# Kernel tuning notes

Measured on AMD Instinct MI355X. Metric: run time of the kernel, lower is better.

## Reference

```python
import jax, jax.numpy as jnp
import numpy as np
import math

E = 64    # d_model = 2*feats
FF = 16   # dim_feedforward
F = 32    # feats
W = 100   # window_size
B = 128   # batch
NH = 32   # nhead = feats


def _mha(q_in, kv_in, w_qkv, b_qkv, w_o, b_o):
    # PyTorch nn.MultiheadAttention, seq-first layout [L, B, E]
    wq, wk, wv = jnp.split(w_qkv, 3, axis=0)
    bq, bk, bv = jnp.split(b_qkv, 3)
    q = q_in @ wq.T + bq
    k = kv_in @ wk.T + bk
    v = kv_in @ wv.T + bv
    L, Bb, _ = q.shape
    S = k.shape[0]
    hd = E // NH  # head_dim = 2
    qh = q.reshape(L, Bb, NH, hd)
    kh = k.reshape(S, Bb, NH, hd)
    vh = v.reshape(S, Bb, NH, hd)
    scores = jnp.einsum('lbhd,sbhd->bhls', qh, kh) / math.sqrt(hd)
    attn = jax.nn.softmax(scores, axis=-1)
    out = jnp.einsum('bhls,sbhd->lbhd', attn, vh).reshape(L, Bb, E)
    return out @ w_o.T + b_o


def _ffn(x, w1, b1, w2, b2):
    h = x @ w1.T + b1
    # nn.LeakyReLU(True) => negative_slope=True==1.0 => identity activation
    return h @ w2.T + b2


def _pos_encode(x):
    # pe[t,d] = sin(t*div[d]) + cos(t*div[d])  (both added, as in source)
    div = jnp.exp(jnp.arange(E, dtype=x.dtype) * (-math.log(10000.0) / E))
    pos = jnp.arange(x.shape[0], dtype=x.dtype)[:, None]
    pe = jnp.sin(pos * div) + jnp.cos(pos * div)  # [W, E]
    return x + pe[:, None, :]


def _encode(src, c, tgt, enc_p):
    (qkv_w, qkv_b, out_w, out_b, l1_w, l1_b, l2_w, l2_b) = enc_p
    s = jnp.concatenate([src, c], axis=2) * math.sqrt(F)
    s = _pos_encode(s)
    s = s + _mha(s, s, qkv_w, qkv_b, out_w, out_b)
    s = s + _ffn(s, l1_w, l1_b, l2_w, l2_b)
    t = jnp.tile(tgt, (1, 1, 2))
    return t, s


def _decode(t, mem, dec_p):
    (sa_qkv_w, sa_qkv_b, sa_out_w, sa_out_b,
     ca_qkv_w, ca_qkv_b, ca_out_w, ca_out_b,
     l1_w, l1_b, l2_w, l2_b) = dec_p
    t = t + _mha(t, t, sa_qkv_w, sa_qkv_b, sa_out_w, sa_out_b)
    t = t + _mha(t, mem, ca_qkv_w, ca_qkv_b, ca_out_w, ca_out_b)
    t = t + _ffn(t, l1_w, l1_b, l2_w, l2_b)
    return t


def _forward(src, tgt,
             enc_qkv_w, enc_qkv_b, enc_out_w, enc_out_b, enc_l1_w, enc_l1_b, enc_l2_w, enc_l2_b,
             d1_sa_qkv_w, d1_sa_qkv_b, d1_sa_out_w, d1_sa_out_b,
             d1_ca_qkv_w, d1_ca_qkv_b, d1_ca_out_w, d1_ca_out_b,
             d1_l1_w, d1_l1_b, d1_l2_w, d1_l2_b,
             d2_sa_qkv_w, d2_sa_qkv_b, d2_sa_out_w, d2_sa_out_b,
             d2_ca_qkv_w, d2_ca_qkv_b, d2_ca_out_w, d2_ca_out_b,
             d2_l1_w, d2_l1_b, d2_l2_w, d2_l2_b,
             fcn_w, fcn_b):
    enc_p = (enc_qkv_w, enc_qkv_b, enc_out_w, enc_out_b, enc_l1_w, enc_l1_b, enc_l2_w, enc_l2_b)
    d1_p = (d1_sa_qkv_w, d1_sa_qkv_b, d1_sa_out_w, d1_sa_out_b,
            d1_ca_qkv_w, d1_ca_qkv_b, d1_ca_out_w, d1_ca_out_b,
            d1_l1_w, d1_l1_b, d1_l2_w, d1_l2_b)
    d2_p = (d2_sa_qkv_w, d2_sa_qkv_b, d2_sa_out_w, d2_sa_out_b,
            d2_ca_qkv_w, d2_ca_qkv_b, d2_ca_out_w, d2_ca_out_b,
            d2_l1_w, d2_l1_b, d2_l2_w, d2_l2_b)
    fcn = lambda x: jax.nn.sigmoid(x @ fcn_w.T + fcn_b)

    c = jnp.zeros_like(src)
    t, mem = _encode(src, c, tgt, enc_p)
    x1 = fcn(_decode(t, mem, d1_p))
    c = (x1 - src) ** 2
    t, mem = _encode(src, c, tgt, enc_p)
    x2 = fcn(_decode(t, mem, d2_p))
    return x1, x2


def setup_inputs() -> dict:
    keys = jax.random.split(jax.random.key(0), 40)
    ki = iter(keys)

    def rn(shape, s=0.05):
        return jax.random.normal(next(ki), shape, dtype=jnp.float32) * s

    inp = {}
    inp['src'] = jax.random.normal(next(ki), (W, B, F), dtype=jnp.float32)
    inp['tgt'] = jax.random.normal(next(ki), (W, B, F), dtype=jnp.float32)
    for pfx in ['enc_', 'd1_sa_', 'd1_ca_', 'd2_sa_', 'd2_ca_']:
        inp[pfx + 'qkv_w'] = rn((3 * E, E))
        inp[pfx + 'qkv_b'] = rn((3 * E,))
        inp[pfx + 'out_w'] = rn((E, E))
        inp[pfx + 'out_b'] = rn((E,))
    for pfx in ['enc_', 'd1_', 'd2_']:
        inp[pfx + 'l1_w'] = rn((FF, E))
        inp[pfx + 'l1_b'] = rn((FF,))
        inp[pfx + 'l2_w'] = rn((E, FF))
        inp[pfx + 'l2_b'] = rn((E,))
    inp['fcn_w'] = rn((F, E))
    inp['fcn_b'] = rn((F,))
    return inp


def reference(src, tgt,
              enc_qkv_w, enc_qkv_b, enc_out_w, enc_out_b, enc_l1_w, enc_l1_b, enc_l2_w, enc_l2_b,
              d1_sa_qkv_w, d1_sa_qkv_b, d1_sa_out_w, d1_sa_out_b,
              d1_ca_qkv_w, d1_ca_qkv_b, d1_ca_out_w, d1_ca_out_b,
              d1_l1_w, d1_l1_b, d1_l2_w, d1_l2_b,
              d2_sa_qkv_w, d2_sa_qkv_b, d2_sa_out_w, d2_sa_out_b,
              d2_ca_qkv_w, d2_ca_qkv_b, d2_ca_out_w, d2_ca_out_b,
              d2_l1_w, d2_l1_b, d2_l2_w, d2_l2_b,
              fcn_w, fcn_b):
    return _forward(src, tgt,
                    enc_qkv_w, enc_qkv_b, enc_out_w, enc_out_b, enc_l1_w, enc_l1_b, enc_l2_w, enc_l2_b,
                    d1_sa_qkv_w, d1_sa_qkv_b, d1_sa_out_w, d1_sa_out_b,
                    d1_ca_qkv_w, d1_ca_qkv_b, d1_ca_out_w, d1_ca_out_b,
                    d1_l1_w, d1_l1_b, d1_l2_w, d1_l2_b,
                    d2_sa_qkv_w, d2_sa_qkv_b, d2_sa_out_w, d2_sa_out_b,
                    d2_ca_qkv_w, d2_ca_qkv_b, d2_ca_out_w, d2_ca_out_b,
                    d2_l1_w, d2_l1_b, d2_l2_w, d2_l2_b,
                    fcn_w, fcn_b)
```

## Files before the change

### kernel.cpp

```cpp
#include <hip/hip_runtime.h>
#include <math.h>


#define TPB 1024
#define RH 50
#define SQ32 5.656854249492381f

#ifndef __has_builtin
#define __has_builtin(x) 0
#endif
#if __has_builtin(__builtin_amdgcn_exp2f)
#define EXP2(x) __builtin_amdgcn_exp2f(x)
#else
#define EXP2(x) exp2f(x)
#endif

typedef float v2f __attribute__((ext_vector_type(2)));
typedef float v4f __attribute__((ext_vector_type(4)));

struct KParams { const void* p[36]; };

template<int K, int MC, int WP>
__device__ __forceinline__ void ldwp(const float* __restrict__ Wt, float* __restrict__ Ws,
                                     int moff, int tid)
{
    for (int i = tid; i < MC * K; i += TPB) {
        int m = i / K, k = i - m * K;
        Ws[k * WP + moff + m] = Wt[i];
    }
}

template<int K, int WP>
__device__ __forceinline__ void gemm_dual24(const float* __restrict__ x0,
                                            const float* __restrict__ x1,
                                            const float* __restrict__ w, v2f acc[4])
{
#pragma unroll 4
    for (int kk = 0; kk < K / 4; ++kk) {
        v4f xa = *reinterpret_cast<const v4f*>(x0 + 4 * kk);
        v4f xb = *reinterpret_cast<const v4f*>(x1 + 4 * kk);
#pragma unroll
        for (int j = 0; j < 4; ++j) {
            v4f wv = *reinterpret_cast<const v4f*>(w + (size_t)(4 * kk + j) * WP);
            v2f xj = {xa[j], xb[j]};
#pragma unroll
            for (int c = 0; c < 4; ++c) {
                v2f wc = {wv[c], wv[c]};
                acc[c] = __builtin_elementwise_fma(xj, wc, acc[c]);
            }
        }
    }
}

template<int K, int WP>
__device__ __forceinline__ void gemm14v(const float* __restrict__ x,
                                        const float* __restrict__ w, float acc[4])
{
#pragma unroll 4
    for (int kk = 0; kk < K / 4; ++kk) {
        v4f xv = *reinterpret_cast<const v4f*>(x + 4 * kk);
#pragma unroll
        for (int j = 0; j < 4; ++j) {
            v4f wv = *reinterpret_cast<const v4f*>(w + (size_t)(4 * kk + j) * WP);
#pragma unroll
            for (int c = 0; c < 4; ++c) acc[c] = fmaf(xv[j], wv[c], acc[c]);
        }
    }
}

__device__ __forceinline__ void kv_gemm(const float* __restrict__ Xkv,
    const float* __restrict__ RW, const float* __restrict__ Bqkv,
    int b, int base, float4* __restrict__ KVs, float4* __restrict__ Gx, int tid)
{
    if (tid >= 800) return;
    const int isV = tid >= 400;
    const int u = tid - (isV ? 400 : 0);
    const int r0 = u >> 4, cg = u & 15;
    v2f acc[4] = {};
    gemm_dual24<64, 132>(Xkv + r0 * 68, Xkv + (r0 + 25) * 68,
                         RW + (isV ? 64 : 0) + 4 * cg, acc);
    v4f bb = *reinterpret_cast<const v4f*>(Bqkv + (isV ? 128 : 64) + 4 * cg);
    const int h0 = 2 * cg;
    const int off = isV ? 2 : 0;
#pragma unroll
    for (int rr = 0; rr < 2; ++rr) {
        int sg = base + r0 + 25 * rr;
        v2f p0 = {acc[0][rr] + bb[0], acc[1][rr] + bb[1]};
        v2f p1 = {acc[2][rr] + bb[2], acc[3][rr] + bb[3]};
        *reinterpret_cast<v2f*>(reinterpret_cast<float*>(KVs + h0 * 101 + sg) + off) = p0;
        *reinterpret_cast<v2f*>(reinterpret_cast<float*>(KVs + (h0 + 1) * 101 + sg) + off) = p1;
        float* g0 = reinterpret_cast<float*>(Gx + ((size_t)b * 100 + sg) * 32 + h0) + off;
        float* g1 = reinterpret_cast<float*>(Gx + ((size_t)b * 100 + sg) * 32 + h0 + 1) + off;
        asm volatile("global_store_dwordx2 %0, %1, off sc0 sc1" :: "v"(g0), "v"(p0) : "memory");
        asm volatile("global_store_dwordx2 %0, %1, off sc0 sc1" :: "v"(g1), "v"(p1) : "memory");
    }
}

__device__ __forceinline__ void flag_pub(int* flagme, int st, int tid)
{
    asm volatile("s_waitcnt vmcnt(0)" ::: "memory");
    __syncthreads();
    if (tid == 0)
        asm volatile("global_store_dword %0, %1, off sc0 sc1" :: "v"(flagme), "v"(st) : "memory");
}

__device__ __forceinline__ void q_gemm(const float* __restrict__ Xq,
    const float* __restrict__ RW, const float* __restrict__ Bqkv,
    float* __restrict__ Q, int tid)
{
    if (tid >= 400) return;
    const int r0 = tid >> 4, cg = tid & 15;
    v2f acc[4] = {};
    gemm_dual24<64, 132>(Xq + r0 * 68, Xq + (r0 + 25) * 68, RW + 4 * cg, acc);
    v4f bb = *reinterpret_cast<const v4f*>(Bqkv + 4 * cg);
#pragma unroll
    for (int rr = 0; rr < 2; ++rr)
        *reinterpret_cast<v4f*>(Q + (r0 + 25 * rr) * 68 + 4 * cg) =
            (v4f){acc[0][rr] + bb[0], acc[1][rr] + bb[1],
                  acc[2][rr] + bb[2], acc[3][rr] + bb[3]};
}

__device__ __forceinline__ void kv_wait(const int* flagpt, int st,
    const float4* __restrict__ Gx, int b, int pbase,
    float4* __restrict__ KVs, int tid)
{
    if (tid == 0) {
        int f;
        for (;;) {
            asm volatile("global_load_dword %0, %1, off sc0 sc1\n\ts_waitcnt vmcnt(0)"
                         : "=v"(f) : "v"(flagpt) : "memory");
            if (f >= st) break;
            __builtin_amdgcn_s_sleep(8);
        }
    }
    __syncthreads();
    const int i2 = tid + 1024;
    v4f a1, a2;
    const float4* p1 = Gx + ((size_t)b * 100 + pbase + (tid >> 5)) * 32 + (tid & 31);
    asm volatile("global_load_dwordx4 %0, %1, off sc0 sc1" : "=v"(a1) : "v"(p1) : "memory");
    if (i2 < 1600) {
        const float4* p2 = Gx + ((size_t)b * 100 + pbase + (i2 >> 5)) * 32 + (i2 & 31);
        asm volatile("global_load_dwordx4 %0, %1, off sc0 sc1" : "=v"(a2) : "v"(p2) : "memory");
    }
    asm volatile("s_waitcnt vmcnt(0)" ::: "memory");
    *reinterpret_cast<v4f*>(KVs + (tid & 31) * 101 + pbase + (tid >> 5)) = a1;
    if (i2 < 1600)
        *reinterpret_cast<v4f*>(KVs + (i2 & 31) * 101 + pbase + (i2 >> 5)) = a2;
    __syncthreads();
}

__device__ __forceinline__ void attn_block(float* __restrict__ Q,
                                           const float4* __restrict__ KVs, int tid)
{
    if (tid < 832) {
        const int u = tid >> 1, sh = tid & 1;
        const int h = u / 13;
        const int g = u - 13 * h;
        const int lq0 = 4 * g;
        const float4* kv = KVs + h * 101 + sh * 50;
        const float SCALE = 0.7071067811865476f * 1.4426950408889634f;
        float q0[4], q1[4];
#pragma unroll
        for (int j = 0; j < 4; ++j) {
            if (lq0 + j < RH) {
                float2 qv = *reinterpret_cast<const float2*>(Q + (lq0 + j) * 68 + 2 * h);
                q0[j] = qv.x * SCALE; q1[j] = qv.y * SCALE;
            } else { q0[j] = 0.f; q1[j] = 0.f; }
        }
        float mx[4] = {-1e30f, -1e30f, -1e30f, -1e30f};
#pragma unroll 5
        for (int s = 0; s < 50; ++s) {
            float4 k = kv[s];
#pragma unroll
            for (int j = 0; j < 4; ++j)
                mx[j] = fmaxf(mx[j], fmaf(q0[j], k.x, q1[j] * k.y));
        }
        float sum[4] = {0, 0, 0, 0}, a0[4] = {0, 0, 0, 0}, a1[4] = {0, 0, 0, 0};
#pragma unroll 5
        for (int s = 0; s < 50; ++s) {
            float4 k = kv[s];
#pragma unroll
            for (int j = 0; j < 4; ++j) {
                float e = EXP2(fmaf(q0[j], k.x, fmaf(q1[j], k.y, -mx[j])));
                sum[j] += e;
                a0[j] = fmaf(e, k.z, a0[j]);
                a1[j] = fmaf(e, k.w, a1[j]);
            }
        }
#pragma unroll
        for (int j = 0; j < 4; ++j) {
            float mo = __shfl_xor(mx[j], 1);
            float so = __shfl_xor(sum[j], 1);
            float ao = __shfl_xor(a0[j], 1);
            float bo = __shfl_xor(a1[j], 1);
            float m = fmaxf(mx[j], mo);
            float c1 = EXP2(mx[j] - m), c2 = EXP2(mo - m);
            float S = fmaf(sum[j], c1, so * c2);
            float A = fmaf(a0[j], c1, ao * c2);
            float B = fmaf(a1[j], c1, bo * c2);
            if (sh == 0 && lq0 + j < RH) {
                float inv = 1.f / S;
                *reinterpret_cast<float2*>(Q + (lq0 + j) * 68 + 2 * h) =
                    make_float2(A * inv, B * inv);
            }
        }
    }
}

__device__ __forceinline__ void out_res(const float* __restrict__ Ain,
    const float* __restrict__ RW, const float* __restrict__ Bi,
    float* __restrict__ Sres, int tid)
{
    if (tid >= 400) return;
    const int r0 = tid >> 4, cg = tid & 15;
    v2f acc[4] = {};
    gemm_dual24<64, 132>(Ain + r0 * 68, Ain + (r0 + 25) * 68, RW + 4 * cg, acc);
    v4f bb = *reinterpret_cast<const v4f*>(Bi + 4 * cg);
#pragma unroll
    for (int rr = 0; rr < 2; ++rr) {
        float* sp = Sres + (r0 + 25 * rr) * 68 + 4 * cg;
        v4f s0 = *reinterpret_cast<v4f*>(sp);
        *reinterpret_cast<v4f*>(sp) =
            (v4f){acc[0][rr] + bb[0] + s0[0], acc[1][rr] + bb[1] + s0[1],
                  acc[2][rr] + bb[2] + s0[2], acc[3][rr] + bb[3] + s0[3]};
    }
}

__global__ __launch_bounds__(TPB) void k_fused(KParams prm, float* __restrict__ outp,
    float4* __restrict__ kvx0, float4* __restrict__ kvx1, int* __restrict__ flags)
{
    __shared__ float R0[RH * 68];
    __shared__ float R1[RH * 68];
    __shared__ float R3[RH * 68];
    __shared__ float4 KVs[32 * 101];
    __shared__ float RW[64 * 132];
    __shared__ float Hs[RH * 20];
    __shared__ float X1s[RH * 36];

    const int tid = threadIdx.x;
    const int b = blockIdx.x & 127;
    const int half = blockIdx.x >> 7;
    const int base = half * RH;
    const int pbase = RH - base;
    int* flagme = flags + (b * 2 + half) * 32;
    int* flagpt = flags + (b * 2 + 1 - half) * 32;

    const float* src = (const float*)prm.p[0];
    const float* tgt = (const float*)prm.p[1];

#define ATT_STAGE(Xq, Xkv, WQKV, BQ, WOUT, BO, SRES, st)                     \
    {                                                                        \
        float4* Gx = ((st) & 1) ? kvx1 : kvx0;                               \
        __syncthreads();                             \
        ldwp<64, 64, 132>((WQKV) + 4096, RW, 0, tid);           \
        ldwp<64, 64, 132>((WQKV) + 8192, RW, 64, tid);          \
        __syncthreads();                                                     \
        kv_gemm(Xkv, RW, BQ, b, base, KVs, Gx, tid);                         \
        flag_pub(flagme, st, tid);               \
        ldwp<64, 64, 132>(WQKV, RW, 0, tid);                    \
        __syncthreads();                                                     \
        q_gemm(Xq, RW, BQ, R1, tid);                                         \
        kv_wait(flagpt, st, Gx, b, pbase, KVs, tid);                         \
        attn_block(R1, KVs, tid);                                            \
        __syncthreads();                                                     \
        ldwp<64, 64, 132>(WOUT, RW, 0, tid);                                 \
        __syncthreads();                                                     \
        out_res(R1, RW, BO, SRES, tid);                                      \
    }

#define FFN_STAGE(X, W1, B1, W2, B2)                                         \
    {                                                                        \
        __syncthreads();                               \
        ldwp<64, 16, 20>(W1, RW, 0, tid);                                    \
        __syncthreads();                                                     \
        if (tid < 800) {                \
            const int r = tid >> 4, c = tid & 15;                            \
            float a = (B1)[c];                                               \
            const float* xrow = (X) + r * 68;                                \
            _Pragma("unroll 4")                                              \
            for (int kk = 0; kk < 16; ++kk) {                                \
                v4f xv = *reinterpret_cast<const v4f*>(xrow + 4 * kk);       \
                _Pragma("unroll")                                            \
                for (int j = 0; j < 4; ++j)                                  \
                    a = fmaf(xv[j], RW[(4 * kk + j) * 20 + c], a);           \
            }                                                                \
            Hs[r * 20 + c] = a;                                              \
        }                                                                    \
        __syncthreads();                                                     \
        ldwp<16, 64, 68>(W2, RW, 0, tid);                                    \
        __syncthreads();                                                     \
        if (tid < 400) {                                                     \
            const int r0 = tid >> 4, cg = tid & 15;                          \
            v2f acc[4] = {};                                                 \
            gemm_dual24<16, 68>(Hs + r0 * 20, Hs + (r0 + 25) * 20,           \
                                RW + 4 * cg, acc);                           \
            v4f bb = *reinterpret_cast<const v4f*>((B2) + 4 * cg);           \
            _Pragma("unroll")                                                \
            for (int rr = 0; rr < 2; ++rr) {                                 \
                float* xp = (X) + (r0 + 25 * rr) * 68 + 4 * cg;              \
                v4f u = *reinterpret_cast<v4f*>(xp);                         \
                *reinterpret_cast<v4f*>(xp) =                                \
                    (v4f){acc[0][rr] + bb[0] + u[0], acc[1][rr] + bb[1] + u[1], \
                          acc[2][rr] + bb[2] + u[2], acc[3][rr] + bb[3] + u[3]}; \
            }                                                                \
        }                                                                    \
        __syncthreads();                                                     \
    }

    for (int pass = 0; pass < 2; ++pass) {
        const float* Wq_enc = (const float*)prm.p[2];
        const float* Beq    = (const float*)prm.p[3];
        const float* Wo_enc = (const float*)prm.p[4];
        const float* Beo    = (const float*)prm.p[5];
        const float* Wel1   = (const float*)prm.p[22];
        const float* Bel1   = (const float*)prm.p[23];
        const float* Wel2   = (const float*)prm.p[24];
        const float* Bel2   = (const float*)prm.p[25];
        const float* Wsa    = (const float*)prm.p[pass ? 14 : 6];
        const float* Bsa    = (const float*)prm.p[pass ? 15 : 7];
        const float* Wsao   = (const float*)prm.p[pass ? 16 : 8];
        const float* Bsao   = (const float*)prm.p[pass ? 17 : 9];
        const float* Wca    = (const float*)prm.p[pass ? 18 : 10];
        const float* Bca    = (const float*)prm.p[pass ? 19 : 11];
        const float* Wcao   = (const float*)prm.p[pass ? 20 : 12];
        const float* Bcao   = (const float*)prm.p[pass ? 21 : 13];
        const float* Wdl1   = (const float*)prm.p[pass ? 30 : 26];
        const float* Bdl1   = (const float*)prm.p[pass ? 31 : 27];
        const float* Wdl2   = (const float*)prm.p[pass ? 32 : 28];
        const float* Bdl2   = (const float*)prm.p[pass ? 33 : 29];
        const float* Wf     = (const float*)prm.p[34];
        const float* Bf     = (const float*)prm.p[35];
        float* outx = outp + (pass ? 409600 : 0);

        __syncthreads();
        for (int i = tid; i < RH * 64; i += TPB) {
            int l = i >> 6, d = i & 63;
            int lg = base + l;
            float sv = src[((size_t)lg * 128 + b) * 32 + (d & 31)];
            float v;
            if (d < 32) v = sv;
            else if (pass == 0) v = 0.f;
            else { float df = X1s[l * 36 + (d - 32)] - sv; v = df * df; }
            float div = __expf((float)d * -0.14391156831212787f);
            float pe = 1.4142135623730951f * __sinf((float)lg * div + 0.7853981633974483f);
            R0[l * 68 + d] = v * SQ32 + pe;
        }
        for (int i = tid; i < RH * 8; i += TPB) {
            int l = i >> 3, q4 = i & 7;
            int lg = base + l;
            float4 tv = *reinterpret_cast<const float4*>(tgt + ((size_t)lg * 128 + b) * 32 + 4 * q4);
            *reinterpret_cast<float4*>(R3 + l * 68 + 4 * q4) = tv;
            *reinterpret_cast<float4*>(R3 + l * 68 + 32 + 4 * q4) = tv;
        }

        ATT_STAGE(R0, R0, Wq_enc, Beq, Wo_enc, Beo, R0, pass * 3 + 1)
        FFN_STAGE(R0, Wel1, Bel1, Wel2, Bel2)

        ATT_STAGE(R3, R3, Wsa, Bsa, Wsao, Bsao, R3, pass * 3 + 2)

        ATT_STAGE(R3, R0, Wca, Bca, Wcao, Bcao, R3, pass * 3 + 3)
        FFN_STAGE(R3, Wdl1, Bdl1, Wdl2, Bdl2)

        ldwp<64, 32, 36>(Wf, RW, 0, tid);
        __syncthreads();
        if (tid < 400) {
            const int r = tid >> 3, lp = tid & 7;
            float a[4] = {0, 0, 0, 0};
            gemm14v<64, 36>(R3 + r * 68, RW + 4 * lp, a);
            v4f bb = *reinterpret_cast<const v4f*>(Bf + 4 * lp);
            v4f o;
#pragma unroll
            for (int c = 0; c < 4; ++c) o[c] = 1.f / (1.f + __expf(-(a[c] + bb[c])));
            int rg = base + r;
            *reinterpret_cast<v4f*>(outx + ((size_t)rg * 128 + b) * 32 + 4 * lp) = o;
            if (pass == 0)
                *reinterpret_cast<v4f*>(X1s + r * 36 + 4 * lp) = o;
        }
    }
#undef ATT_STAGE
#undef FFN_STAGE
}

extern "C" void kernel_launch(void* const* d_in, const int* in_sizes, int n_in,
                              void* d_out, int out_size, void* d_ws, size_t ws_size,
                              hipStream_t stream)
{
    KParams prm;
    for (int i = 0; i < 36; ++i) prm.p[i] = d_in[i];
    float4* kvx0 = (float4*)d_ws;
    float4* kvx1 = kvx0 + 409600;
    int* flags = (int*)(kvx1 + 409600);
    k_fused<<<dim3(256), dim3(TPB), 0, stream>>>(prm, (float*)d_out, kvx0, kvx1, flags);
}
```

Baseline: 182.6 us.

## Prefetch next-stage weights into registers and stage them through a second LDS buffer

Weight matrices for each stage are now read from global memory into per-thread registers one stage ahead. The loads are issued during the preceding attention or FFN work, so their latency overlaps compute and the blocking global-load-then-sync sequence disappears. A second shared buffer (RW2) holds the Q and output-projection weights, which lets fewer barriers separate the KV, Q and out-projection GEMMs. The out-projection weights are stored while waiting on the partner block's KV flag. The cost is extra registers and LDS per block, and the code is more rigid because it hardcodes 1024 threads to 4096-element weight tiles.

```diff
diff --git a/kernel.cpp b/kernel.cpp
--- a/kernel.cpp
+++ b/kernel.cpp
@@ -20,13 +20,17 @@
 
 struct KParams { const void* p[36]; };
 
-template<int K, int MC, int WP>
-__device__ __forceinline__ void ldwp(const float* __restrict__ Wt, float* __restrict__ Ws,
-                                     int moff, int tid)
-{
-    for (int i = tid; i < MC * K; i += TPB) {
-        int m = i / K, k = i - m * K;
-        Ws[k * WP + moff + m] = Wt[i];
+__device__ __forceinline__ v4f ld4(const float* __restrict__ W, int tid)
+{
+    return *reinterpret_cast<const v4f*>(W + 4 * tid);
+}
+template<int WP>
+__device__ __forceinline__ void st64x64(v4f w, float* __restrict__ Ws, int moff, int tid)
+{
+#pragma unroll
+    for (int j = 0; j < 4; ++j) {
+        int i = 4 * tid + j, m = i >> 6, k = i & 63;
+        Ws[k * WP + moff + m] = w[j];
     }
 }
 
@@ -105,13 +109,13 @@
 }
 
 __device__ __forceinline__ void q_gemm(const float* __restrict__ Xq,
-    const float* __restrict__ RW, const float* __restrict__ Bqkv,
+    const float* __restrict__ RW2, const float* __restrict__ Bqkv,
     float* __restrict__ Q, int tid)
 {
     if (tid >= 400) return;
     const int r0 = tid >> 4, cg = tid & 15;
     v2f acc[4] = {};
-    gemm_dual24<64, 132>(Xq + r0 * 68, Xq + (r0 + 25) * 68, RW + 4 * cg, acc);
+    gemm_dual24<64, 68>(Xq + r0 * 68, Xq + (r0 + 25) * 68, RW2 + 4 * cg, acc);
     v4f bb = *reinterpret_cast<const v4f*>(Bqkv + 4 * cg);
 #pragma unroll
     for (int rr = 0; rr < 2; ++rr)
@@ -208,13 +212,13 @@
 }
 
 __device__ __forceinline__ void out_res(const float* __restrict__ Ain,
-    const float* __restrict__ RW, const float* __restrict__ Bi,
+    const float* __restrict__ RW2, const float* __restrict__ Bi,
     float* __restrict__ Sres, int tid)
 {
     if (tid >= 400) return;
     const int r0 = tid >> 4, cg = tid & 15;
     v2f acc[4] = {};
-    gemm_dual24<64, 132>(Ain + r0 * 68, Ain + (r0 + 25) * 68, RW + 4 * cg, acc);
+    gemm_dual24<64, 68>(Ain + r0 * 68, Ain + (r0 + 25) * 68, RW2 + 4 * cg, acc);
     v4f bb = *reinterpret_cast<const v4f*>(Bi + 4 * cg);
 #pragma unroll
     for (int rr = 0; rr < 2; ++rr) {
@@ -234,6 +238,7 @@
     __shared__ float R3[RH * 68];
     __shared__ float4 KVs[32 * 101];
     __shared__ float RW[64 * 132];
+    __shared__ float RW2[64 * 68];
     __shared__ float Hs[RH * 20];
     __shared__ float X1s[RH * 36];
 
@@ -248,63 +253,23 @@
     const float* src = (const float*)prm.p[0];
     const float* tgt = (const float*)prm.p[1];
 
-#define ATT_STAGE(Xq, Xkv, WQKV, BQ, WOUT, BO, SRES, st)                     \
-    {                                                                        \
-        float4* Gx = ((st) & 1) ? kvx1 : kvx0;                               \
-        __syncthreads();                             \
-        ldwp<64, 64, 132>((WQKV) + 4096, RW, 0, tid);           \
-        ldwp<64, 64, 132>((WQKV) + 8192, RW, 64, tid);          \
-        __syncthreads();                                                     \
-        kv_gemm(Xkv, RW, BQ, b, base, KVs, Gx, tid);                         \
-        flag_pub(flagme, st, tid);               \
-        ldwp<64, 64, 132>(WQKV, RW, 0, tid);                    \
-        __syncthreads();                                                     \
-        q_gemm(Xq, RW, BQ, R1, tid);                                         \
-        kv_wait(flagpt, st, Gx, b, pbase, KVs, tid);                         \
-        attn_block(R1, KVs, tid);                                            \
-        __syncthreads();                                                     \
-        ldwp<64, 64, 132>(WOUT, RW, 0, tid);                                 \
-        __syncthreads();                                                     \
-        out_res(R1, RW, BO, SRES, tid);                                      \
-    }
-
-#define FFN_STAGE(X, W1, B1, W2, B2)                                         \
-    {                                                                        \
-        __syncthreads();                               \
-        ldwp<64, 16, 20>(W1, RW, 0, tid);                                    \
-        __syncthreads();                                                     \
-        if (tid < 800) {                \
-            const int r = tid >> 4, c = tid & 15;                            \
-            float a = (B1)[c];                                               \
-            const float* xrow = (X) + r * 68;                                \
-            _Pragma("unroll 4")                                              \
-            for (int kk = 0; kk < 16; ++kk) {                                \
-                v4f xv = *reinterpret_cast<const v4f*>(xrow + 4 * kk);       \
-                _Pragma("unroll")                                            \
-                for (int j = 0; j < 4; ++j)                                  \
-                    a = fmaf(xv[j], RW[(4 * kk + j) * 20 + c], a);           \
-            }                                                                \
-            Hs[r * 20 + c] = a;                                              \
-        }                                                                    \
-        __syncthreads();                                                     \
-        ldwp<16, 64, 68>(W2, RW, 0, tid);                                    \
-        __syncthreads();                                                     \
-        if (tid < 400) {                                                     \
-            const int r0 = tid >> 4, cg = tid & 15;                          \
-            v2f acc[4] = {};                                                 \
-            gemm_dual24<16, 68>(Hs + r0 * 20, Hs + (r0 + 25) * 20,           \
-                                RW + 4 * cg, acc);                           \
-            v4f bb = *reinterpret_cast<const v4f*>((B2) + 4 * cg);           \
-            _Pragma("unroll")                                                \
-            for (int rr = 0; rr < 2; ++rr) {                                 \
-                float* xp = (X) + (r0 + 25 * rr) * 68 + 4 * cg;              \
-                v4f u = *reinterpret_cast<v4f*>(xp);                         \
-                *reinterpret_cast<v4f*>(xp) =                                \
-                    (v4f){acc[0][rr] + bb[0] + u[0], acc[1][rr] + bb[1] + u[1], \
-                          acc[2][rr] + bb[2] + u[2], acc[3][rr] + bb[3] + u[3]}; \
-            }                                                                \
-        }                                                                    \
-        __syncthreads();                                                     \
+#define ATT_STAGE(Xq, Xkv, BQ, BO, SRES, st, PRE)                        \
+    {                                                                    \
+        float4* Gx = ((st) & 1) ? kvx1 : kvx0;                           \
+        __syncthreads();               \
+        st64x64<132>(wK, RW, 0, tid);                                    \
+        st64x64<132>(wV, RW, 64, tid);                                   \
+        st64x64<68>(wQ, RW2, 0, tid);                                    \
+        __syncthreads();                                                 \
+        kv_gemm(Xkv, RW, BQ, b, base, KVs, Gx, tid);                     \
+        flag_pub(flagme, st, tid);           \
+        q_gemm(Xq, RW2, BQ, R1, tid);                                    \
+        kv_wait(flagpt, st, Gx, b, pbase, KVs, tid);                     \
+        st64x64<68>(wOut, RW2, 0, tid);       \
+        PRE;                                                             \
+        attn_block(R1, KVs, tid);                                        \
+        __syncthreads();                                                 \
+        out_res(R1, RW2, BO, SRES, tid);                                 \
     }
 
     for (int pass = 0; pass < 2; ++pass) {
@@ -332,6 +297,12 @@
         const float* Bf     = (const float*)prm.p[35];
         float* outx = outp + (pass ? 409600 : 0);
 
+        v4f wK = ld4(Wq_enc + 4096, tid);
+        v4f wV = ld4(Wq_enc + 8192, tid);
+        v4f wQ = ld4(Wq_enc, tid);
+        v4f wOut = ld4(Wo_enc, tid);
+        float f1, f2, h0, h1;
+
         __syncthreads();
         for (int i = tid; i < RH * 64; i += TPB) {
             int l = i >> 6, d = i & 63;
@@ -353,20 +324,98 @@
             *reinterpret_cast<float4*>(R3 + l * 68 + 32 + 4 * q4) = tv;
         }
 
-        ATT_STAGE(R0, R0, Wq_enc, Beq, Wo_enc, Beo, R0, pass * 3 + 1)
-        FFN_STAGE(R0, Wel1, Bel1, Wel2, Bel2)
-
-        ATT_STAGE(R3, R3, Wsa, Bsa, Wsao, Bsao, R3, pass * 3 + 2)
-
-        ATT_STAGE(R3, R0, Wca, Bca, Wcao, Bcao, R3, pass * 3 + 3)
-        FFN_STAGE(R3, Wdl1, Bdl1, Wdl2, Bdl2)
-
-        ldwp<64, 32, 36>(Wf, RW, 0, tid);
+        ATT_STAGE(R0, R0, Beq, Beo, R0, pass * 3 + 1,
+                  (f1 = Wel1[tid], f2 = Wel2[tid]))
+
+        {
+            __syncthreads();
+            { int m = tid >> 6, k = tid & 63; RW[k * 20 + m] = f1; }
+            { int m = tid >> 4, k = tid & 15; RW2[k * 68 + m] = f2; }
+            __syncthreads();
+            if (tid < 800) {
+                const int r = tid >> 4, c = tid & 15;
+                float a = Bel1[c];
+                const float* xrow = R0 + r * 68;
+#pragma unroll 4
+                for (int kk = 0; kk < 16; ++kk) {
+                    v4f xv = *reinterpret_cast<const v4f*>(xrow + 4 * kk);
+#pragma unroll
+                    for (int j = 0; j < 4; ++j)
+                        a = fmaf(xv[j], RW[(4 * kk + j) * 20 + c], a);
+                }
+                Hs[r * 20 + c] = a;
+            }
+            wK = ld4(Wsa + 4096, tid);
+            wV = ld4(Wsa + 8192, tid);
+            wQ = ld4(Wsa, tid);
+            wOut = ld4(Wsao, tid);
+            __syncthreads();
+            if (tid < 400) {
+                const int r0 = tid >> 4, cg = tid & 15;
+                v2f acc[4] = {};
+                gemm_dual24<16, 68>(Hs + r0 * 20, Hs + (r0 + 25) * 20, RW2 + 4 * cg, acc);
+                v4f bb = *reinterpret_cast<const v4f*>(Bel2 + 4 * cg);
+#pragma unroll
+                for (int rr = 0; rr < 2; ++rr) {
+                    float* xp = R0 + (r0 + 25 * rr) * 68 + 4 * cg;
+                    v4f u = *reinterpret_cast<v4f*>(xp);
+                    *reinterpret_cast<v4f*>(xp) =
+                        (v4f){acc[0][rr] + bb[0] + u[0], acc[1][rr] + bb[1] + u[1],
+                              acc[2][rr] + bb[2] + u[2], acc[3][rr] + bb[3] + u[3]};
+                }
+            }
+        }
+
+        ATT_STAGE(R3, R3, Bsa, Bsao, R3, pass * 3 + 2,
+                  (wK = ld4(Wca + 4096, tid), wV = ld4(Wca + 8192, tid),
+                   wQ = ld4(Wca, tid), wOut = ld4(Wcao, tid)))
+
+        ATT_STAGE(R3, R0, Bca, Bcao, R3, pass * 3 + 3,
+                  (f1 = Wdl1[tid], f2 = Wdl2[tid],
+                   h0 = Wf[tid], h1 = Wf[tid + 1024]))
+
+        {
+            __syncthreads();
+            { int m = tid >> 6, k = tid & 63; RW[k * 20 + m] = f1; }
+            { int m = tid >> 4, k = tid & 15; RW2[k * 68 + m] = f2; }
+            { int m = tid >> 6, k = tid & 63; RW[1280 + k * 36 + m] = h0; }
+            { int i2 = tid + 1024, m = i2 >> 6, k = i2 & 63; RW[1280 + k * 36 + m] = h1; }
+            __syncthreads();
+            if (tid < 800) {
+                const int r = tid >> 4, c = tid & 15;
+                float a = Bdl1[c];
+                const float* xrow = R3 + r * 68;
+#pragma unroll 4
+                for (int kk = 0; kk < 16; ++kk) {
+                    v4f xv = *reinterpret_cast<const v4f*>(xrow + 4 * kk);
+#pragma unroll
+                    for (int j = 0; j < 4; ++j)
+                        a = fmaf(xv[j], RW[(4 * kk + j) * 20 + c], a);
+                }
+                Hs[r * 20 + c] = a;
+            }
+            __syncthreads();
+            if (tid < 400) {
+                const int r0 = tid >> 4, cg = tid & 15;
+                v2f acc[4] = {};
+                gemm_dual24<16, 68>(Hs + r0 * 20, Hs + (r0 + 25) * 20, RW2 + 4 * cg, acc);
+                v4f bb = *reinterpret_cast<const v4f*>(Bdl2 + 4 * cg);
+#pragma unroll
+                for (int rr = 0; rr < 2; ++rr) {
+                    float* xp = R3 + (r0 + 25 * rr) * 68 + 4 * cg;
+                    v4f u = *reinterpret_cast<v4f*>(xp);
+                    *reinterpret_cast<v4f*>(xp) =
+                        (v4f){acc[0][rr] + bb[0] + u[0], acc[1][rr] + bb[1] + u[1],
+                              acc[2][rr] + bb[2] + u[2], acc[3][rr] + bb[3] + u[3]};
+                }
+            }
+        }
+
         __syncthreads();
         if (tid < 400) {
             const int r = tid >> 3, lp = tid & 7;
             float a[4] = {0, 0, 0, 0};
-            gemm14v<64, 36>(R3 + r * 68, RW + 4 * lp, a);
+            gemm14v<64, 36>(R3 + r * 68, RW + 1280 + 4 * lp, a);
             v4f bb = *reinterpret_cast<const v4f*>(Bf + 4 * lp);
             v4f o;
 #pragma unroll
@@ -378,7 +427,6 @@
         }
     }
 #undef ATT_STAGE
-#undef FFN_STAGE
 }
 
 extern "C" void kernel_launch(void* const* d_in, const int* in_sizes, int n_in,
```

Measured after the change: 188.5 us. +3.3%, slower.

## Split each batch sequence across four blocks instead of two

Applied to the files above, without the earlier changes.

Each batch element's 100-token window now goes to four 512-thread blocks of 25 rows, up from two 1024-thread blocks of 50 rows, so 512 blocks launch instead of 256. Every block publishes its K/V rows to global memory, waits on the flags of the other three blocks, and pulls the full K/V in two 16-head halves to keep shared memory small. The attention reduction now merges four key slices with a two-step shuffle, and the dual-row GEMM helper is replaced by a single-row one. This spreads work over more CUs at the cost of more cross-block flag waits, more global K/V traffic, and extra barriers.

```diff
diff --git a/kernel.cpp b/kernel.cpp
--- a/kernel.cpp
+++ b/kernel.cpp
@@ -2,8 +2,8 @@
 #include <math.h>
 
 
-#define TPB 1024
-#define RH 50
+#define TPB 512
+#define RH 25
 #define SQ32 5.656854249492381f
 
 #ifndef __has_builtin
@@ -21,34 +21,11 @@
 struct KParams { const void* p[36]; };
 
 template<int K, int MC, int WP>
-__device__ __forceinline__ void ldwp(const float* __restrict__ Wt, float* __restrict__ Ws,
-                                     int moff, int tid)
+__device__ __forceinline__ void ldwp(const float* __restrict__ Wt, float* __restrict__ Ws, int tid)
 {
     for (int i = tid; i < MC * K; i += TPB) {
         int m = i / K, k = i - m * K;
-        Ws[k * WP + moff + m] = Wt[i];
-    }
-}
-
-template<int K, int WP>
-__device__ __forceinline__ void gemm_dual24(const float* __restrict__ x0,
-                                            const float* __restrict__ x1,
-                                            const float* __restrict__ w, v2f acc[4])
-{
-#pragma unroll 4
-    for (int kk = 0; kk < K / 4; ++kk) {
-        v4f xa = *reinterpret_cast<const v4f*>(x0 + 4 * kk);
-        v4f xb = *reinterpret_cast<const v4f*>(x1 + 4 * kk);
-#pragma unroll
-        for (int j = 0; j < 4; ++j) {
-            v4f wv = *reinterpret_cast<const v4f*>(w + (size_t)(4 * kk + j) * WP);
-            v2f xj = {xa[j], xb[j]};
-#pragma unroll
-            for (int c = 0; c < 4; ++c) {
-                v2f wc = {wv[c], wv[c]};
-                acc[c] = __builtin_elementwise_fma(xj, wc, acc[c]);
-            }
-        }
+        Ws[k * WP + m] = Wt[i];
     }
 }
 
@@ -68,32 +45,22 @@
     }
 }
 
-__device__ __forceinline__ void kv_gemm(const float* __restrict__ Xkv,
-    const float* __restrict__ RW, const float* __restrict__ Bqkv,
-    int b, int base, float4* __restrict__ KVs, float4* __restrict__ Gx, int tid)
-{
-    if (tid >= 800) return;
-    const int isV = tid >= 400;
-    const int u = tid - (isV ? 400 : 0);
-    const int r0 = u >> 4, cg = u & 15;
-    v2f acc[4] = {};
-    gemm_dual24<64, 132>(Xkv + r0 * 68, Xkv + (r0 + 25) * 68,
-                         RW + (isV ? 64 : 0) + 4 * cg, acc);
+__device__ __forceinline__ void kv_chunk(const float* __restrict__ X,
+    const float* __restrict__ RW, const float* __restrict__ Bqkv, int isV,
+    int b, int base, float4* __restrict__ Gx, int tid)
+{
+    if (tid >= 400) return;
+    const int r = tid >> 4, cg = tid & 15;
+    float a[4] = {0, 0, 0, 0};
+    gemm14v<64, 68>(X + r * 68, RW + 4 * cg, a);
     v4f bb = *reinterpret_cast<const v4f*>(Bqkv + (isV ? 128 : 64) + 4 * cg);
-    const int h0 = 2 * cg;
-    const int off = isV ? 2 : 0;
-#pragma unroll
-    for (int rr = 0; rr < 2; ++rr) {
-        int sg = base + r0 + 25 * rr;
-        v2f p0 = {acc[0][rr] + bb[0], acc[1][rr] + bb[1]};
-        v2f p1 = {acc[2][rr] + bb[2], acc[3][rr] + bb[3]};
-        *reinterpret_cast<v2f*>(reinterpret_cast<float*>(KVs + h0 * 101 + sg) + off) = p0;
-        *reinterpret_cast<v2f*>(reinterpret_cast<float*>(KVs + (h0 + 1) * 101 + sg) + off) = p1;
-        float* g0 = reinterpret_cast<float*>(Gx + ((size_t)b * 100 + sg) * 32 + h0) + off;
-        float* g1 = reinterpret_cast<float*>(Gx + ((size_t)b * 100 + sg) * 32 + h0 + 1) + off;
-        asm volatile("global_store_dwordx2 %0, %1, off sc0 sc1" :: "v"(g0), "v"(p0) : "memory");
-        asm volatile("global_store_dwordx2 %0, %1, off sc0 sc1" :: "v"(g1), "v"(p1) : "memory");
-    }
+    const int sg = base + r, h0 = 2 * cg, off = isV ? 2 : 0;
+    v2f p0 = {a[0] + bb[0], a[1] + bb[1]};
+    v2f p1 = {a[2] + bb[2], a[3] + bb[3]};
+    float* g0 = reinterpret_cast<float*>(Gx + ((size_t)b * 100 + sg) * 32 + h0) + off;
+    float* g1 = reinterpret_cast<float*>(Gx + ((size_t)b * 100 + sg) * 32 + h0 + 1) + off;
+    asm volatile("global_store_dwordx2 %0, %1, off sc0 sc1" :: "v"(g0), "v"(p0) : "memory");
+    asm volatile("global_store_dwordx2 %0, %1, off sc0 sc1" :: "v"(g1), "v"(p1) : "memory");
 }
 
 __device__ __forceinline__ void flag_pub(int* flagme, int st, int tid)
@@ -109,67 +76,78 @@
     float* __restrict__ Q, int tid)
 {
     if (tid >= 400) return;
-    const int r0 = tid >> 4, cg = tid & 15;
-    v2f acc[4] = {};
-    gemm_dual24<64, 132>(Xq + r0 * 68, Xq + (r0 + 25) * 68, RW + 4 * cg, acc);
+    const int r = tid >> 4, cg = tid & 15;
+    float a[4] = {0, 0, 0, 0};
+    gemm14v<64, 68>(Xq + r * 68, RW + 4 * cg, a);
     v4f bb = *reinterpret_cast<const v4f*>(Bqkv + 4 * cg);
-#pragma unroll
-    for (int rr = 0; rr < 2; ++rr)
-        *reinterpret_cast<v4f*>(Q + (r0 + 25 * rr) * 68 + 4 * cg) =
-            (v4f){acc[0][rr] + bb[0], acc[1][rr] + bb[1],
-                  acc[2][rr] + bb[2], acc[3][rr] + bb[3]};
-}
-
-__device__ __forceinline__ void kv_wait(const int* flagpt, int st,
-    const float4* __restrict__ Gx, int b, int pbase,
-    float4* __restrict__ KVs, int tid)
+    *reinterpret_cast<v4f*>(Q + r * 68 + 4 * cg) =
+        (v4f){a[0] + bb[0], a[1] + bb[1], a[2] + bb[2], a[3] + bb[3]};
+}
+
+__device__ __forceinline__ void wait3(const int* __restrict__ flags, int b, int q,
+                                      int st, int tid)
 {
     if (tid == 0) {
-        int f;
-        for (;;) {
-            asm volatile("global_load_dword %0, %1, off sc0 sc1\n\ts_waitcnt vmcnt(0)"
-                         : "=v"(f) : "v"(flagpt) : "memory");
-            if (f >= st) break;
-            __builtin_amdgcn_s_sleep(8);
+#pragma unroll
+        for (int j = 1; j < 4; ++j) {
+            const int* fp = flags + (b * 4 + ((q + j) & 3)) * 32;
+            int f;
+            for (;;) {
+                asm volatile("global_load_dword %0, %1, off sc0 sc1\n\ts_waitcnt vmcnt(0)"
+                             : "=v"(f) : "v"(fp) : "memory");
+                if (f >= st) break;
+                __builtin_amdgcn_s_sleep(8);
+            }
         }
     }
     __syncthreads();
-    const int i2 = tid + 1024;
-    v4f a1, a2;
-    const float4* p1 = Gx + ((size_t)b * 100 + pbase + (tid >> 5)) * 32 + (tid & 31);
+}
+
+__device__ __forceinline__ void kv_pull(const float4* __restrict__ Gx, int b, int p,
+                                        float4* __restrict__ KVh, int tid)
+{
+    const int s = tid >> 4, hl = tid & 15;
+    const float4* B0 = Gx + (size_t)b * 3200 + p * 16 + hl;
+    v4f a0, a1, a2, a3 = {0, 0, 0, 0};
+    const float4* p0 = B0 + (size_t)s * 32;
+    const float4* p1 = B0 + (size_t)(s + 32) * 32;
+    const float4* p2 = B0 + (size_t)(s + 64) * 32;
+    asm volatile("global_load_dwordx4 %0, %1, off sc0 sc1" : "=v"(a0) : "v"(p0) : "memory");
     asm volatile("global_load_dwordx4 %0, %1, off sc0 sc1" : "=v"(a1) : "v"(p1) : "memory");
-    if (i2 < 1600) {
-        const float4* p2 = Gx + ((size_t)b * 100 + pbase + (i2 >> 5)) * 32 + (i2 & 31);
-        asm volatile("global_load_dwordx4 %0, %1, off sc0 sc1" : "=v"(a2) : "v"(p2) : "memory");
+    asm volatile("global_load_dwordx4 %0, %1, off sc0 sc1" : "=v"(a2) : "v"(p2) : "memory");
+    if (s < 4) {
+        const float4* p3 = B0 + (size_t)(s + 96) * 32;
+        asm volatile("global_load_dwordx4 %0, %1, off sc0 sc1" : "=v"(a3) : "v"(p3) : "memory");
     }
     asm volatile("s_waitcnt vmcnt(0)" ::: "memory");
-    *reinterpret_cast<v4f*>(KVs + (tid & 31) * 101 + pbase + (tid >> 5)) = a1;
-    if (i2 < 1600)
-        *reinterpret_cast<v4f*>(KVs + (i2 & 31) * 101 + pbase + (i2 >> 5)) = a2;
-    __syncthreads();
-}
-
-__device__ __forceinline__ void attn_block(float* __restrict__ Q,
-                                           const float4* __restrict__ KVs, int tid)
-{
-    if (tid < 832) {
-        const int u = tid >> 1, sh = tid & 1;
-        const int h = u / 13;
-        const int g = u - 13 * h;
-        const int lq0 = 4 * g;
-        const float4* kv = KVs + h * 101 + sh * 50;
+    *reinterpret_cast<v4f*>(KVh + hl * 101 + s) = a0;
+    *reinterpret_cast<v4f*>(KVh + hl * 101 + s + 32) = a1;
+    *reinterpret_cast<v4f*>(KVh + hl * 101 + s + 64) = a2;
+    if (s < 4)
+        *reinterpret_cast<v4f*>(KVh + hl * 101 + s + 96) = a3;
+}
+
+__device__ __forceinline__ void attn_part(float* __restrict__ Q,
+    const float4* __restrict__ KVh, int p, int tid)
+{
+    if (tid < 448) {
+        const int ks = tid & 3, u = tid >> 2;
+        const int h = u / 7, qg = u - 7 * h;
+        const int lq0 = 4 * qg;
+        const int hg = p * 16 + h;
+        const float4* kv = KVh + h * 101 + ks * 25;
         const float SCALE = 0.7071067811865476f * 1.4426950408889634f;
         float q0[4], q1[4];
 #pragma unroll
         for (int j = 0; j < 4; ++j) {
             if (lq0 + j < RH) {
-                float2 qv = *reinterpret_cast<const float2*>(Q + (lq0 + j) * 68 + 2 * h);
+                float2 qv = *reinterpret_cast<const float2*>(Q + (lq0 + j) * 68 + 2 * hg);
                 q0[j] = qv.x * SCALE; q1[j] = qv.y * SCALE;
             } else { q0[j] = 0.f; q1[j] = 0.f; }
         }
         float mx[4] = {-1e30f, -1e30f, -1e30f, -1e30f};
 #pragma unroll 5
-        for (int s = 0; s < 50; ++s) {
+        for (int s = 0; s < 25; ++s) {
             float4 k = kv[s];
 #pragma unroll
             for (int j = 0; j < 4; ++j)
@@ -177,7 +155,7 @@
         }
         float sum[4] = {0, 0, 0, 0}, a0[4] = {0, 0, 0, 0}, a1[4] = {0, 0, 0, 0};
 #pragma unroll 5
-        for (int s = 0; s < 50; ++s) {
+        for (int s = 0; s < 25; ++s) {
             float4 k = kv[s];
 #pragma unroll
             for (int j = 0; j < 4; ++j) {
@@ -189,19 +167,23 @@
         }
 #pragma unroll
         for (int j = 0; j < 4; ++j) {
-            float mo = __shfl_xor(mx[j], 1);
-            float so = __shfl_xor(sum[j], 1);
-            float ao = __shfl_xor(a0[j], 1);
-            float bo = __shfl_xor(a1[j], 1);
-            float m = fmaxf(mx[j], mo);
-            float c1 = EXP2(mx[j] - m), c2 = EXP2(mo - m);
-            float S = fmaf(sum[j], c1, so * c2);
-            float A = fmaf(a0[j], c1, ao * c2);
-            float B = fmaf(a1[j], c1, bo * c2);
-            if (sh == 0 && lq0 + j < RH) {
-                float inv = 1.f / S;
-                *reinterpret_cast<float2*>(Q + (lq0 + j) * 68 + 2 * h) =
-                    make_float2(A * inv, B * inv);
+#pragma unroll
+            for (int d = 1; d <= 2; d <<= 1) {
+                float mo = __shfl_xor(mx[j], d);
+                float so = __shfl_xor(sum[j], d);
+                float ao = __shfl_xor(a0[j], d);
+                float bo = __shfl_xor(a1[j], d);
+                float M = fmaxf(mx[j], mo);
+                float c1 = EXP2(mx[j] - M), c2 = EXP2(mo - M);
+                sum[j] = fmaf(sum[j], c1, so * c2);
+                a0[j] = fmaf(a0[j], c1, ao * c2);
+                a1[j] = fmaf(a1[j], c1, bo * c2);
+                mx[j] = M;
+            }
+            if (ks == 0 && lq0 + j < RH) {
+                float inv = 1.f / sum[j];
+                *reinterpret_cast<float2*>(Q + (lq0 + j) * 68 + 2 * hg) =
+                    make_float2(a0[j] * inv, a1[j] * inv);
             }
         }
     }
@@ -212,38 +194,33 @@
     float* __restrict__ Sres, int tid)
 {
     if (tid >= 400) return;
-    const int r0 = tid >> 4, cg = tid & 15;
-    v2f acc[4] = {};
-    gemm_dual24<64, 132>(Ain + r0 * 68, Ain + (r0 + 25) * 68, RW + 4 * cg, acc);
+    const int r = tid >> 4, cg = tid & 15;
+    float a[4] = {0, 0, 0, 0};
+    gemm14v<64, 68>(Ain + r * 68, RW + 4 * cg, a);
     v4f bb = *reinterpret_cast<const v4f*>(Bi + 4 * cg);
-#pragma unroll
-    for (int rr = 0; rr < 2; ++rr) {
-        float* sp = Sres + (r0 + 25 * rr) * 68 + 4 * cg;
-        v4f s0 = *reinterpret_cast<v4f*>(sp);
-        *reinterpret_cast<v4f*>(sp) =
-            (v4f){acc[0][rr] + bb[0] + s0[0], acc[1][rr] + bb[1] + s0[1],
-                  acc[2][rr] + bb[2] + s0[2], acc[3][rr] + bb[3] + s0[3]};
-    }
-}
-
-__global__ __launch_bounds__(TPB) void k_fused(KParams prm, float* __restrict__ outp,
+    float* sp = Sres + r * 68 + 4 * cg;
+    v4f s0 = *reinterpret_cast<v4f*>(sp);
+    *reinterpret_cast<v4f*>(sp) =
+        (v4f){a[0] + bb[0] + s0[0], a[1] + bb[1] + s0[1],
+              a[2] + bb[2] + s0[2], a[3] + bb[3] + s0[3]};
+}
+
+__global__ __launch_bounds__(TPB, 4) void k_fused(KParams prm, float* __restrict__ outp,
     float4* __restrict__ kvx0, float4* __restrict__ kvx1, int* __restrict__ flags)
 {
     __shared__ float R0[RH * 68];
     __shared__ float R1[RH * 68];
     __shared__ float R3[RH * 68];
-    __shared__ float4 KVs[32 * 101];
-    __shared__ float RW[64 * 132];
+    __shared__ float4 KVh[16 * 101];
+    __shared__ float RW[64 * 68];
     __shared__ float Hs[RH * 20];
     __shared__ float X1s[RH * 36];
 
     const int tid = threadIdx.x;
-    const int b = blockIdx.x & 127;
-    const int half = blockIdx.x >> 7;
-    const int base = half * RH;
-    const int pbase = RH - base;
-    int* flagme = flags + (b * 2 + half) * 32;
-    int* flagpt = flags + (b * 2 + 1 - half) * 32;
+    const int b = blockIdx.x >> 2;
+    const int q = blockIdx.x & 3;
+    const int base = q * RH;
+    int* flagme = flags + (b * 4 + q) * 32;
 
     const float* src = (const float*)prm.p[0];
     const float* tgt = (const float*)prm.p[1];
@@ -252,18 +229,26 @@
     {                                                                        \
         float4* Gx = ((st) & 1) ? kvx1 : kvx0;                               \
         __syncthreads();                             \
-        ldwp<64, 64, 132>((WQKV) + 4096, RW, 0, tid);           \
-        ldwp<64, 64, 132>((WQKV) + 8192, RW, 64, tid);          \
-        __syncthreads();                                                     \
-        kv_gemm(Xkv, RW, BQ, b, base, KVs, Gx, tid);                         \
+        ldwp<64, 64, 68>((WQKV) + 4096, RW, tid);             \
+        __syncthreads();                                                     \
+        kv_chunk(Xkv, RW, BQ, 0, b, base, Gx, tid);                          \
+        __syncthreads();                                                     \
+        ldwp<64, 64, 68>((WQKV) + 8192, RW, tid);             \
+        __syncthreads();                                                     \
+        kv_chunk(Xkv, RW, BQ, 1, b, base, Gx, tid);                          \
         flag_pub(flagme, st, tid);               \
-        ldwp<64, 64, 132>(WQKV, RW, 0, tid);                    \
+        ldwp<64, 64, 68>(WQKV, RW, tid);                      \
         __syncthreads();                                                     \
         q_gemm(Xq, RW, BQ, R1, tid);                                         \
-        kv_wait(flagpt, st, Gx, b, pbase, KVs, tid);                         \
-        attn_block(R1, KVs, tid);                                            \
-        __syncthreads();                                                     \
-        ldwp<64, 64, 132>(WOUT, RW, 0, tid);                                 \
+        wait3(flags, b, q, st, tid);                                         \
+        kv_pull(Gx, b, 0, KVh, tid);                                         \
+        __syncthreads();                                                     \
+        attn_part(R1, KVh, 0, tid);                                          \
+        __syncthreads();                                      \
+        kv_pull(Gx, b, 1, KVh, tid);                                         \
+        __syncthreads();                                                     \
+        attn_part(R1, KVh, 1, tid);                                          \
+        ldwp<64, 64, 68>(WOUT, RW, tid);           \
         __syncthreads();                                                     \
         out_res(R1, RW, BO, SRES, tid);                                      \
     }
@@ -271,9 +256,9 @@
 #define FFN_STAGE(X, W1, B1, W2, B2)                                         \
     {                                                                        \
         __syncthreads();                               \
-        ldwp<64, 16, 20>(W1, RW, 0, tid);                                    \
-        __syncthreads();                                                     \
-        if (tid < 800) {                \
+        ldwp<64, 16, 20>(W1, RW, tid);                                       \
+        __syncthreads();                                                     \
+        if (tid < 400) {                \
             const int r = tid >> 4, c = tid & 15;                            \
             float a = (B1)[c];                                               \
             const float* xrow = (X) + r * 68;                                \
@@ -287,22 +272,18 @@
             Hs[r * 20 + c] = a;                                              \
         }                                                                    \
         __syncthreads();                                                     \
-        ldwp<16, 64, 68>(W2, RW, 0, tid);                                    \
+        ldwp<16, 64, 68>(W2, RW, tid);                                       \
         __syncthreads();                                                     \
         if (tid < 400) {                                                     \
-            const int r0 = tid >> 4, cg = tid & 15;                          \
-            v2f acc[4] = {};                                                 \
-            gemm_dual24<16, 68>(Hs + r0 * 20, Hs + (r0 + 25) * 20,           \
-                                RW + 4 * cg, acc);                           \
+            const int r = tid >> 4, cg = tid & 15;                           \
+            float a[4] = {0, 0, 0, 0};                                       \
+            gemm14v<16, 68>(Hs + r * 20, RW + 4 * cg, a);                    \
             v4f bb = *reinterpret_cast<const v4f*>((B2) + 4 * cg);           \
-            _Pragma("unroll")                                                \
-            for (int rr = 0; rr < 2; ++rr) {                                 \
-                float* xp = (X) + (r0 + 25 * rr) * 68 + 4 * cg;              \
-                v4f u = *reinterpret_cast<v4f*>(xp);                         \
-                *reinterpret_cast<v4f*>(xp) =                                \
-                    (v4f){acc[0][rr] + bb[0] + u[0], acc[1][rr] + bb[1] + u[1], \
-                          acc[2][rr] + bb[2] + u[2], acc[3][rr] + bb[3] + u[3]}; \
-            }                                                                \
+            float* xp = (X) + r * 68 + 4 * cg;                               \
+            v4f u = *reinterpret_cast<v4f*>(xp);                             \
+            *reinterpret_cast<v4f*>(xp) =                                    \
+                (v4f){a[0] + bb[0] + u[0], a[1] + bb[1] + u[1],              \
+                      a[2] + bb[2] + u[2], a[3] + bb[3] + u[3]};             \
         }                                                                    \
         __syncthreads();                                                     \
     }
@@ -361,9 +342,9 @@
         ATT_STAGE(R3, R0, Wca, Bca, Wcao, Bcao, R3, pass * 3 + 3)
         FFN_STAGE(R3, Wdl1, Bdl1, Wdl2, Bdl2)
 
-        ldwp<64, 32, 36>(Wf, RW, 0, tid);
+        ldwp<64, 32, 36>(Wf, RW, tid);
         __syncthreads();
-        if (tid < 400) {
+        if (tid < 200) {
             const int r = tid >> 3, lp = tid & 7;
             float a[4] = {0, 0, 0, 0};
             gemm14v<64, 36>(R3 + r * 68, RW + 4 * lp, a);
@@ -390,5 +371,5 @@
     float4* kvx0 = (float4*)d_ws;
     float4* kvx1 = kvx0 + 409600;
     int* flags = (int*)(kvx1 + 409600);
-    k_fused<<<dim3(256), dim3(TPB), 0, stream>>>(prm, (float*)d_out, kvx0, kvx1, flags);
-}
+    k_fused<<<dim3(512), dim3(TPB), 0, stream>>>(prm, (float*)d_out, kvx0, kvx1, flags);
+}
```

Measured after the change: 240.3 us. 1.32x slower.
